# Kernel tuning notes

Measured on AMD Instinct MI355X. Metric: run time of the kernel, lower is better.

Reference implementation:

```python
import jax, jax.numpy as jnp
import numpy as np

VOCAB = 3149
T_MAX = 256
C = 128      # n_emb
H = 8        # n_heads
D = C // H   # head_size = 16
L = 6        # n blocks
FF = 4 * C
EPS = 1e-5


def _layernorm(x, g, b):
    mu = jnp.mean(x, axis=-1, keepdims=True)
    var = jnp.mean((x - mu) ** 2, axis=-1, keepdims=True)
    return (x - mu) / jnp.sqrt(var + EPS) * g + b


def setup_inputs() -> dict:
    key = jax.random.key(0)
    ks = jax.random.split(key, 24)
    s = 0.02
    inp = {
        "tokens": jax.random.randint(ks[0], (64, 256), 0, VOCAB),
        "tok_emb": jax.random.normal(ks[1], (VOCAB, C), jnp.float32) * s,
        "pos_emb": jax.random.normal(ks[2], (T_MAX, C), jnp.float32) * s,
        "Wq": jax.random.normal(ks[3], (L, H, C, D), jnp.float32) * s,
        "Wk": jax.random.normal(ks[4], (L, H, C, D), jnp.float32) * s,
        "Wv": jax.random.normal(ks[5], (L, H, C, D), jnp.float32) * s,
        "Wproj": jax.random.normal(ks[6], (L, C, C), jnp.float32) * s,
        "bproj": jnp.zeros((L, C), jnp.float32),
        "ln1_g": jnp.ones((L, C), jnp.float32),
        "ln1_b": jnp.zeros((L, C), jnp.float32),
        "ln2_g": jnp.ones((L, C), jnp.float32),
        "ln2_b": jnp.zeros((L, C), jnp.float32),
        "W1": jax.random.normal(ks[7], (L, C, FF), jnp.float32) * s,
        "b1": jnp.zeros((L, FF), jnp.float32),
        "W2": jax.random.normal(ks[8], (L, FF, C), jnp.float32) * s,
        "b2": jnp.zeros((L, C), jnp.float32),
        "lnf_g": jnp.ones((C,), jnp.float32),
        "lnf_b": jnp.zeros((C,), jnp.float32),
        "Wlm": jax.random.normal(ks[9], (C, VOCAB), jnp.float32) * s,
        "blm": jnp.zeros((VOCAB,), jnp.float32),
    }
    return inp


def reference(tokens, tok_emb, pos_emb, Wq, Wk, Wv, Wproj, bproj,
              ln1_g, ln1_b, ln2_g, ln2_b, W1, b1, W2, b2,
              lnf_g, lnf_b, Wlm, blm):
    B, T = tokens.shape
    x = tok_emb[tokens] + pos_emb[:T][None, :, :]  # (B,T,C)
    # NOTE: original code scales scores by C**-0.5 with C = n_emb (128), not head_size.
    scale = jnp.asarray(C, x.dtype) ** -0.5
    causal = jnp.tril(jnp.ones((T, T), bool))
    neg_inf = jnp.asarray(-jnp.inf, x.dtype)
    for l in range(L):
        xn = _layernorm(x, ln1_g[l], ln1_b[l])
        q = jnp.einsum('btc,hcd->bhtd', xn, Wq[l])
        k = jnp.einsum('btc,hcd->bhtd', xn, Wk[l])
        v = jnp.einsum('btc,hcd->bhtd', xn, Wv[l])
        wei = jnp.einsum('bhtd,bhsd->bhts', q, k) * scale
        wei = jnp.where(causal[None, None], wei, neg_inf)
        wei = jax.nn.softmax(wei, axis=-1)
        attn = jnp.einsum('bhts,bhsd->bhtd', wei, v)
        attn = attn.transpose(0, 2, 1, 3).reshape(B, T, C)  # concat heads
        x = x + jnp.einsum('btc,cf->btf', attn, Wproj[l]) + bproj[l]
        xn2 = _layernorm(x, ln2_g[l], ln2_b[l])
        h = jax.nn.relu(jnp.einsum('btc,cf->btf', xn2, W1[l]) + b1[l])
        x = x + jnp.einsum('btf,fc->btc', h, W2[l]) + b2[l]
    x = _layernorm(x, lnf_g, lnf_b)
    logits = jnp.einsum('btc,cv->btv', x, Wlm) + blm
    return logits
```

## Files before the change

kernel.cpp:

```cpp
#include <hip/hip_runtime.h>
#include <hip/hip_bf16.h>
#include <math.h>

#define BT   16384
#define CDIM 128
#define TSEQ 256
#define NBAT 64
#define NH   8
#define HD   16
#define NL   6
#define FFD  512
#define NV   3149

typedef __bf16 bfv8 __attribute__((ext_vector_type(8)));
typedef float  fv4  __attribute__((ext_vector_type(4)));
typedef short  s4   __attribute__((ext_vector_type(4)));
typedef unsigned short u16;
typedef unsigned int   u32;
typedef u16 u16v8 __attribute__((ext_vector_type(8)));

__device__ __forceinline__ u16 f2b(float f) {
  u32 u = __builtin_bit_cast(u32, f);
  u += 0x7FFFu + ((u >> 16) & 1u);
  return (u16)(u >> 16);
}
__device__ __forceinline__ u32 cvtpk(float lo, float hi) {
  u32 r;
  asm("v_cvt_pk_bf16_f32 %0, %1, %2" : "=v"(r) : "v"(lo), "v"(hi));
  return r;
}
__device__ __forceinline__ fv4 mfma16(s4 a, s4 b, fv4 c) {
#if __has_builtin(__builtin_amdgcn_mfma_f32_16x16x16bf16_1k)
  return __builtin_amdgcn_mfma_f32_16x16x16bf16_1k(a, b, c, 0, 0, 0);
#else
  fv4 d;
  asm volatile("v_mfma_f32_16x16x16_bf16 %0, %1, %2, %3"
               : "=v"(d) : "v"(a), "v"(b), "v"(c));
  return d;
#endif
}

__global__ __launch_bounds__(256) void embed_kernel(
    const int* __restrict__ tokens, const float* __restrict__ tok_emb,
    const float* __restrict__ pos_emb, float* __restrict__ x) {
  int i4 = blockIdx.x * 256 + threadIdx.x;
  if (i4 >= BT * CDIM / 4) return;
  int i  = i4 * 4;
  int c  = i & (CDIM - 1);
  int bt = i >> 7;
  int t  = bt & (TSEQ - 1);
  int tok = tokens[bt];
  float4 te = *(const float4*)(tok_emb + (size_t)tok * CDIM + c);
  float4 pe = *(const float4*)(pos_emb + (size_t)t * CDIM + c);
  float4 r;
  r.x = te.x + pe.x; r.y = te.y + pe.y; r.z = te.z + pe.z; r.w = te.w + pe.w;
  *(float4*)(x + i) = r;
}

__global__ __launch_bounds__(256) void packqkv_bf16(
    const float* __restrict__ Wq, const float* __restrict__ Wk,
    const float* __restrict__ Wv, u16* __restrict__ dst) {
  int idx = blockIdx.x * 256 + threadIdx.x;
  if (idx >= NL * 384 * CDIM) return;
  int c = idx & 127;
  int j = (idx >> 7) % 384;
  int l = idx / (384 * CDIM);
  int sel = j >> 7;
  int jj  = j & 127;
  int h   = jj >> 4;
  int d   = jj & 15;
  const float* W = (sel == 0) ? Wq : (sel == 1) ? Wk : Wv;
  dst[idx] = f2b(W[(((size_t)l * NH + h) * CDIM + c) * HD + d]);
}

__global__ __launch_bounds__(256) void transpose_cast_t(
    const float* __restrict__ src, u16* __restrict__ dst, int R, int C) {
  __shared__ float tile[32][33];
  int l  = blockIdx.z;
  int r0 = blockIdx.y * 32, c0 = blockIdx.x * 32;
  int tr = threadIdx.x >> 5, tc = threadIdx.x & 31;
  #pragma unroll
  for (int p = 0; p < 4; p++) {
    int r = r0 + tr + p * 8, c = c0 + tc;
    if (r < R && c < C) tile[tr + p * 8][tc] = src[((size_t)l * R + r) * C + c];
  }
  __syncthreads();
  #pragma unroll
  for (int p = 0; p < 4; p++) {
    int c = c0 + tr + p * 8, r = r0 + tc;
    if (r < R && c < C) dst[((size_t)l * C + c) * R + r] = f2b(tile[tc][tr + p * 8]);
  }
}

__global__ __launch_bounds__(256) void ln_kernel(
    const float* __restrict__ x, const float* __restrict__ g,
    const float* __restrict__ b, u16* __restrict__ out) {
  int wid  = blockIdx.x * 4 + (threadIdx.x >> 6);
  int lane = threadIdx.x & 63;
  const float2 v = ((const float2*)(x + (size_t)wid * CDIM))[lane];
  float s = v.x + v.y;
  #pragma unroll
  for (int m = 1; m < 64; m <<= 1) s += __shfl_xor(s, m);
  float mu = s * (1.f / CDIM);
  float dx = v.x - mu, dy = v.y - mu;
  float s2 = dx * dx + dy * dy;
  #pragma unroll
  for (int m = 1; m < 64; m <<= 1) s2 += __shfl_xor(s2, m);
  float rstd = rsqrtf(s2 * (1.f / CDIM) + 1e-5f);
  float2 gg = ((const float2*)g)[lane];
  float2 bb = ((const float2*)b)[lane];
  u32 pack = (u32)f2b(dx * rstd * gg.x + bb.x) |
             ((u32)f2b(dy * rstd * gg.y + bb.y) << 16);
  ((u32*)(out + (size_t)wid * CDIM))[lane] = pack;
}

template<int OMODE, bool BIAS, bool RELU, int BN>
__global__ __launch_bounds__(256) void gemm_mfma(
    const u16* __restrict__ A, const u16* __restrict__ Btp,
    const float* __restrict__ bias, void* __restrict__ Cout,
    int M, int N, int K) {
  constexpr int BM = 128, BK = 32, PAD = 40;
  constexpr int NF = BN / 32;
  __shared__ u16 As[BM][PAD];
  __shared__ u16 Bs[BN][PAD];
  const int tid  = threadIdx.x;
  const int lane = tid & 63;
  const int wv   = tid >> 6;
  const int wm   = wv & 1;
  const int wn   = wv >> 1;
  const int m0 = blockIdx.y * BM;
  const int n0 = blockIdx.x * BN;
  const int srow = tid >> 2;
  const int sk8  = (tid & 3) * 8;
  const int fr = lane & 15;
  const int fk = (lane >> 4) * 8;

  fv4 acc[4][NF];
  #pragma unroll
  for (int i = 0; i < 4; i++)
    #pragma unroll
    for (int j = 0; j < NF; j++) acc[i][j] = (fv4){0.f, 0.f, 0.f, 0.f};

  for (int k0 = 0; k0 < K; k0 += BK) {
    #pragma unroll
    for (int p = 0; p < 2; p++) {
      int r = srow + p * 64;
      *(uint4*)&As[r][sk8] = *(const uint4*)(A + (size_t)(m0 + r) * K + k0 + sk8);
    }
    #pragma unroll
    for (int p = 0; p < BN / 64; p++) {
      int r = srow + p * 64;
      int n = n0 + r;
      uint4 v = make_uint4(0u, 0u, 0u, 0u);
      if (n < N) v = *(const uint4*)(Btp + (size_t)n * K + k0 + sk8);
      *(uint4*)&Bs[r][sk8] = v;
    }
    __syncthreads();
    bfv8 a[4], b[NF];
    #pragma unroll
    for (int i = 0; i < 4; i++)
      a[i] = *(const bfv8*)&As[wm * 64 + i * 16 + fr][fk];
    #pragma unroll
    for (int j = 0; j < NF; j++)
      b[j] = *(const bfv8*)&Bs[wn * (BN / 2) + j * 16 + fr][fk];
    #pragma unroll
    for (int i = 0; i < 4; i++)
      #pragma unroll
      for (int j = 0; j < NF; j++)
        acc[i][j] = __builtin_amdgcn_mfma_f32_16x16x32_bf16(a[i], b[j], acc[i][j], 0, 0, 0);
    __syncthreads();
  }

  const int row0 = m0 + wm * 64;
  const int col0 = n0 + wn * (BN / 2);
  const int lr   = (lane >> 4) * 4;
  #pragma unroll
  for (int j = 0; j < NF; j++) {
    int col = col0 + j * 16 + fr;
    if (col >= N) continue;
    float bz = BIAS ? bias[col] : 0.f;
    #pragma unroll
    for (int i = 0; i < 4; i++) {
      #pragma unroll
      for (int q = 0; q < 4; q++) {
        int row = row0 + i * 16 + lr + q;
        float v = acc[i][j][q] + bz;
        if (RELU) v = fmaxf(v, 0.f);
        if (OMODE == 0)      ((u16*)Cout)[(size_t)row * N + col] = f2b(v);
        else if (OMODE == 1) ((float*)Cout)[(size_t)row * N + col] = v;
        else                 ((float*)Cout)[(size_t)row * N + col] += v;
      }
    }
  }
}

template<bool BIAS, bool RELU>
__global__ __launch_bounds__(256) void gemm_ln_mfma(
    const float* __restrict__ X, const u16* __restrict__ Btp,
    const float* __restrict__ lng, const float* __restrict__ lnb,
    const float* __restrict__ bias, u16* __restrict__ Cout,
    int M, int N) {
  constexpr int BM = 128, BN = 128, BK = 32;
  __shared__ u16 As[BM][136];
  __shared__ u16 Bs[BN][40];
  const int tid  = threadIdx.x;
  const int lane = tid & 63;
  const int wv   = tid >> 6;
  const int wm   = wv & 1;
  const int wn   = wv >> 1;
  const int m0 = blockIdx.y * BM;
  const int n0 = blockIdx.x * BN;
  const int fr = lane & 15;
  const int fk = (lane >> 4) * 8;

  {
    const int l32  = lane & 31;
    const int rsel = lane >> 5;
    float4 gg = *(const float4*)(lng + l32 * 4);
    float4 bb = *(const float4*)(lnb + l32 * 4);
    #pragma unroll 4
    for (int it = 0; it < 16; it++) {
      int r = wv * 32 + it * 2 + rsel;
      float4 v = *(const float4*)(X + (size_t)(m0 + r) * 128 + l32 * 4);
      float s = (v.x + v.y) + (v.z + v.w);
      #pragma unroll
      for (int m = 1; m < 32; m <<= 1) s += __shfl_xor(s, m);
      float mu = s * (1.f / 128.f);
      float dx = v.x - mu, dy = v.y - mu, dz = v.z - mu, dw = v.w - mu;
      float s2 = (dx * dx + dy * dy) + (dz * dz + dw * dw);
      #pragma unroll
      for (int m = 1; m < 32; m <<= 1) s2 += __shfl_xor(s2, m);
      float rstd = rsqrtf(s2 * (1.f / 128.f) + 1e-5f);
      u32 p0 = cvtpk(dx * rstd * gg.x + bb.x, dy * rstd * gg.y + bb.y);
      u32 p1 = cvtpk(dz * rstd * gg.z + bb.z, dw * rstd * gg.w + bb.w);
      *(uint2*)&As[r][l32 * 4] = make_uint2(p0, p1);
    }
  }

  fv4 acc[4][4];
  #pragma unroll
  for (int i = 0; i < 4; i++)
    #pragma unroll
    for (int j = 0; j < 4; j++) acc[i][j] = (fv4){0.f, 0.f, 0.f, 0.f};

  for (int k0 = 0; k0 < 128; k0 += BK) {
    #pragma unroll
    for (int p = 0; p < 2; p++) {
      int ch = tid + p * 256;
      int row = ch >> 2, c8 = (ch & 3) * 8;
      *(uint4*)&Bs[row][c8] = *(const uint4*)(Btp + (size_t)(n0 + row) * 128 + k0 + c8);
    }
    __syncthreads();
    bfv8 a[4], b[4];
    #pragma unroll
    for (int i = 0; i < 4; i++)
      a[i] = *(const bfv8*)&As[wm * 64 + i * 16 + fr][k0 + fk];
    #pragma unroll
    for (int j = 0; j < 4; j++)
      b[j] = *(const bfv8*)&Bs[wn * 64 + j * 16 + fr][fk];
    #pragma unroll
    for (int i = 0; i < 4; i++)
      #pragma unroll
      for (int j = 0; j < 4; j++)
        acc[i][j] = __builtin_amdgcn_mfma_f32_16x16x32_bf16(a[i], b[j], acc[i][j], 0, 0, 0);
    __syncthreads();
  }

  const int row0 = m0 + wm * 64;
  const int col0 = n0 + wn * 64;
  const int lr   = (lane >> 4) * 4;
  #pragma unroll
  for (int j = 0; j < 4; j++) {
    int col = col0 + j * 16 + fr;
    float bz = BIAS ? bias[col] : 0.f;
    #pragma unroll
    for (int i = 0; i < 4; i++) {
      #pragma unroll
      for (int q = 0; q < 4; q++) {
        int row = row0 + i * 16 + lr + q;
        float v = acc[i][j][q] + bz;
        if (RELU) v = fmaxf(v, 0.f);
        Cout[(size_t)row * N + col] = f2b(v);
      }
    }
  }
}

__global__ __launch_bounds__(256) void attn_mfma(
    const u16* __restrict__ qkv, u16* __restrict__ out) {
  const float scale = 0.08838834764831843f;
  __shared__ u16 Qs[128][20];
  __shared__ u16 Ks[TSEQ][20];
  __shared__ u16 Vt[HD][280];
  const int blk = blockIdx.x;
  const int qh = blk & 1;
  const int h  = (blk >> 1) & (NH - 1);
  const int b  = blk >> 4;
  const int tid = threadIdx.x;

  #pragma unroll
  for (int p = 0; p < 2; p++) {
    int idx = tid + p * 256;
    int r  = idx >> 1;
    int c8 = (idx & 1) * 8;
    const u16* base = qkv + (size_t)(b * TSEQ + r) * 384 + h * HD + c8;
    uint4 k  = *(const uint4*)(base + CDIM);
    u16v8 v  = *(const u16v8*)(base + 2 * CDIM);
    *(uint4*)&Ks[r][c8] = k;
    #pragma unroll
    for (int i = 0; i < 8; i++) Vt[c8 + i][r] = v[i];
  }
  {
    int r  = tid >> 1;
    int c8 = (tid & 1) * 8;
    const u16* base = qkv + (size_t)(b * TSEQ + qh * 128 + r) * 384 + h * HD + c8;
    *(uint4*)&Qs[r][c8] = *(const uint4*)(base);
  }
  __syncthreads();

  const int wv   = tid >> 6;
  const int lane = tid & 63;
  const int fr = lane & 15;
  const int g  = lane >> 4;

  #pragma unroll 1
  for (int qi = 0; qi < 2; qi++) {
    const int qt = qh * 8 + (qi ? (7 - wv) : wv);
    const int qr = (qt - qh * 8) * 16 + fr;
    s4 qf = *(const s4*)&Qs[qr][g * 4];

    fv4 sf[16];
    #pragma unroll
    for (int st = 0; st < 16; st++) {
      if (st <= qt) {
        s4 kf = *(const s4*)&Ks[st * 16 + fr][g * 4];
        sf[st] = mfma16(kf, qf, (fv4){0.f, 0.f, 0.f, 0.f});
      }
    }

    float mx = -3.4e38f;
    #pragma unroll
    for (int st = 0; st < 16; st++) {
      if (st <= qt) {
        #pragma unroll
        for (int r = 0; r < 4; r++) {
          float v = sf[st][r] * scale;
          if (st == qt && (4 * g + r) > fr) v = -3.4e38f;
          sf[st][r] = v;
          mx = fmaxf(mx, v);
        }
      }
    }
    mx = fmaxf(mx, __shfl_xor(mx, 16));
    mx = fmaxf(mx, __shfl_xor(mx, 32));

    float sum = 0.f;
    uint2 pk[16];
    #pragma unroll
    for (int st = 0; st < 16; st++) {
      if (st <= qt) {
        float e0 = __expf(sf[st][0] - mx), e1 = __expf(sf[st][1] - mx);
        float e2 = __expf(sf[st][2] - mx), e3 = __expf(sf[st][3] - mx);
        sum += (e0 + e1) + (e2 + e3);
        pk[st] = make_uint2(cvtpk(e0, e1), cvtpk(e2, e3));
      }
    }
    sum += __shfl_xor(sum, 16);
    sum += __shfl_xor(sum, 32);
    const float inv = 1.f / sum;

    fv4 accO = (fv4){0.f, 0.f, 0.f, 0.f};
    #pragma unroll
    for (int st = 0; st < 16; st++) {
      if (st <= qt) {
        s4 vf = *(const s4*)&Vt[fr][st * 16 + g * 4];
        s4 pf = __builtin_bit_cast(s4, pk[st]);
        accO = mfma16(vf, pf, accO);
      }
    }

    const int q_glob = qt * 16 + fr;
    u32 lo = cvtpk(accO[0] * inv, accO[1] * inv);
    u32 hi = cvtpk(accO[2] * inv, accO[3] * inv);
    *(uint2*)(out + (size_t)(b * TSEQ + q_glob) * CDIM + h * HD + 4 * g) =
        make_uint2(lo, hi);
  }
}

extern "C" void kernel_launch(void* const* d_in, const int* in_sizes, int n_in,
                              void* d_out, int out_size, void* d_ws, size_t ws_size,
                              hipStream_t stream) {
  const int*   tokens  = (const int*)  d_in[0];
  const float* tok_emb = (const float*)d_in[1];
  const float* pos_emb = (const float*)d_in[2];
  const float* Wq      = (const float*)d_in[3];
  const float* Wk      = (const float*)d_in[4];
  const float* Wv      = (const float*)d_in[5];
  const float* Wproj   = (const float*)d_in[6];
  const float* bproj   = (const float*)d_in[7];
  const float* ln1_g   = (const float*)d_in[8];
  const float* ln1_b   = (const float*)d_in[9];
  const float* ln2_g   = (const float*)d_in[10];
  const float* ln2_b   = (const float*)d_in[11];
  const float* W1      = (const float*)d_in[12];
  const float* b1      = (const float*)d_in[13];
  const float* W2      = (const float*)d_in[14];
  const float* b2      = (const float*)d_in[15];
  const float* lnf_g   = (const float*)d_in[16];
  const float* lnf_b   = (const float*)d_in[17];
  const float* Wlm     = (const float*)d_in[18];
  const float* blm     = (const float*)d_in[19];
  float* out = (float*)d_out;

  char* W = (char*)d_ws;
  float* x    = (float*)(W);
  u16*   xn   = (u16*)  (W + 8388608);
  u16*   qkvb = (u16*)  (W + 12582912);
  u16*   att  = (u16*)  (W + 25165824);
  u16*   hbuf = (u16*)  (W + 29360128);
  u16*   wqkv = (u16*)  (W + 46137344);
  u16*   wpj  = (u16*)  (W + 46727168);
  u16*   w1t  = (u16*)  (W + 46923776);
  u16*   w2t  = (u16*)  (W + 47710208);
  u16*   wlmt = (u16*)  (W + 48496640);

  packqkv_bf16<<<(NL * 384 * CDIM + 255) / 256, 256, 0, stream>>>(Wq, Wk, Wv, wqkv);
  transpose_cast_t<<<dim3(4, 4, NL), 256, 0, stream>>>(Wproj, wpj, CDIM, CDIM);
  transpose_cast_t<<<dim3(16, 4, NL), 256, 0, stream>>>(W1, w1t, CDIM, FFD);
  transpose_cast_t<<<dim3(4, 16, NL), 256, 0, stream>>>(W2, w2t, FFD, CDIM);
  transpose_cast_t<<<dim3((NV + 31) / 32, 4, 1), 256, 0, stream>>>(Wlm, wlmt, CDIM, NV);
  embed_kernel<<<(BT * CDIM / 4 + 255) / 256, 256, 0, stream>>>(tokens, tok_emb, pos_emb, x);

  for (int l = 0; l < NL; l++) {
    gemm_ln_mfma<false, false><<<dim3(3, BT / 128), 256, 0, stream>>>(
        x, wqkv + (size_t)l * 384 * CDIM, ln1_g + l * CDIM, ln1_b + l * CDIM,
        nullptr, qkvb, BT, 384);
    attn_mfma<<<NBAT * NH * 2, 256, 0, stream>>>(qkvb, att);
    gemm_mfma<2, true, false, 64><<<dim3(2, BT / 128), 256, 0, stream>>>(
        att, wpj + (size_t)l * CDIM * CDIM, bproj + l * CDIM, x, BT, CDIM, CDIM);
    gemm_ln_mfma<true, true><<<dim3(4, BT / 128), 256, 0, stream>>>(
        x, w1t + (size_t)l * FFD * CDIM, ln2_g + l * CDIM, ln2_b + l * CDIM,
        b1 + l * FFD, hbuf, BT, FFD);
    gemm_mfma<2, true, false, 64><<<dim3(2, BT / 128), 256, 0, stream>>>(
        hbuf, w2t + (size_t)l * CDIM * FFD, b2 + l * CDIM, x, BT, CDIM, FFD);
  }
  ln_kernel<<<BT / 4, 256, 0, stream>>>(x, lnf_g, lnf_b, xn);
  gemm_mfma<1, true, false, 128><<<dim3((NV + 127) / 128, BT / 128), 256, 0, stream>>>(
      xn, wlmt, blm, out, BT, NV, CDIM);
}
```

Baseline: 847.4 us.

## Fuse final layernorm into LM head, shrink GEMM row tiles, use online-softmax attention

The final layernorm kernel is removed and folded into the LM-head GEMM through a generalized gemm_ln_mfma that can write float output and handles ragged N. The per-layer GEMMs switch from 128-row to 64-row tiles, doubling the block count for better CU occupancy. Attention replaces the two-pass softmax over a 16-tile score array with a streaming online-softmax loop, which lowers register pressure at the cost of extra rescaling and shuffles per tile. The V-transpose shared array padding is also changed to alter bank mapping.

Measured after the change: 758.3 us. 10.5% less time.

```diff
diff --git a/kernel.cpp b/kernel.cpp
--- a/kernel.cpp
+++ b/kernel.cpp
@@ -92,34 +92,13 @@
   }
 }
 
-__global__ __launch_bounds__(256) void ln_kernel(
-    const float* __restrict__ x, const float* __restrict__ g,
-    const float* __restrict__ b, u16* __restrict__ out) {
-  int wid  = blockIdx.x * 4 + (threadIdx.x >> 6);
-  int lane = threadIdx.x & 63;
-  const float2 v = ((const float2*)(x + (size_t)wid * CDIM))[lane];
-  float s = v.x + v.y;
-  #pragma unroll
-  for (int m = 1; m < 64; m <<= 1) s += __shfl_xor(s, m);
-  float mu = s * (1.f / CDIM);
-  float dx = v.x - mu, dy = v.y - mu;
-  float s2 = dx * dx + dy * dy;
-  #pragma unroll
-  for (int m = 1; m < 64; m <<= 1) s2 += __shfl_xor(s2, m);
-  float rstd = rsqrtf(s2 * (1.f / CDIM) + 1e-5f);
-  float2 gg = ((const float2*)g)[lane];
-  float2 bb = ((const float2*)b)[lane];
-  u32 pack = (u32)f2b(dx * rstd * gg.x + bb.x) |
-             ((u32)f2b(dy * rstd * gg.y + bb.y) << 16);
-  ((u32*)(out + (size_t)wid * CDIM))[lane] = pack;
-}
-
-template<int OMODE, bool BIAS, bool RELU, int BN>
+template<int OMODE, bool BIAS, bool RELU, int BM, int BN>
 __global__ __launch_bounds__(256) void gemm_mfma(
     const u16* __restrict__ A, const u16* __restrict__ Btp,
     const float* __restrict__ bias, void* __restrict__ Cout,
     int M, int N, int K) {
-  constexpr int BM = 128, BK = 32, PAD = 40;
+  constexpr int BK = 32, PAD = 40;
+  constexpr int MI = BM / 32;
   constexpr int NF = BN / 32;
   __shared__ u16 As[BM][PAD];
   __shared__ u16 Bs[BN][PAD];
@@ -135,15 +114,15 @@
   const int fr = lane & 15;
   const int fk = (lane >> 4) * 8;
 
-  fv4 acc[4][NF];
-  #pragma unroll
-  for (int i = 0; i < 4; i++)
+  fv4 acc[MI][NF];
+  #pragma unroll
+  for (int i = 0; i < MI; i++)
     #pragma unroll
     for (int j = 0; j < NF; j++) acc[i][j] = (fv4){0.f, 0.f, 0.f, 0.f};
 
   for (int k0 = 0; k0 < K; k0 += BK) {
     #pragma unroll
-    for (int p = 0; p < 2; p++) {
+    for (int p = 0; p < BM / 64; p++) {
       int r = srow + p * 64;
       *(uint4*)&As[r][sk8] = *(const uint4*)(A + (size_t)(m0 + r) * K + k0 + sk8);
     }
@@ -156,22 +135,22 @@
       *(uint4*)&Bs[r][sk8] = v;
     }
     __syncthreads();
-    bfv8 a[4], b[NF];
-    #pragma unroll
-    for (int i = 0; i < 4; i++)
-      a[i] = *(const bfv8*)&As[wm * 64 + i * 16 + fr][fk];
+    bfv8 a[MI], b[NF];
+    #pragma unroll
+    for (int i = 0; i < MI; i++)
+      a[i] = *(const bfv8*)&As[wm * (BM / 2) + i * 16 + fr][fk];
     #pragma unroll
     for (int j = 0; j < NF; j++)
       b[j] = *(const bfv8*)&Bs[wn * (BN / 2) + j * 16 + fr][fk];
     #pragma unroll
-    for (int i = 0; i < 4; i++)
+    for (int i = 0; i < MI; i++)
       #pragma unroll
       for (int j = 0; j < NF; j++)
         acc[i][j] = __builtin_amdgcn_mfma_f32_16x16x32_bf16(a[i], b[j], acc[i][j], 0, 0, 0);
     __syncthreads();
   }
 
-  const int row0 = m0 + wm * 64;
+  const int row0 = m0 + wm * (BM / 2);
   const int col0 = n0 + wn * (BN / 2);
   const int lr   = (lane >> 4) * 4;
   #pragma unroll
@@ -180,7 +159,7 @@
     if (col >= N) continue;
     float bz = BIAS ? bias[col] : 0.f;
     #pragma unroll
-    for (int i = 0; i < 4; i++) {
+    for (int i = 0; i < MI; i++) {
       #pragma unroll
       for (int q = 0; q < 4; q++) {
         int row = row0 + i * 16 + lr + q;
@@ -194,13 +173,15 @@
   }
 }
 
-template<bool BIAS, bool RELU>
+template<int OMODE, bool BIAS, bool RELU, int BM, int BN>
 __global__ __launch_bounds__(256) void gemm_ln_mfma(
     const float* __restrict__ X, const u16* __restrict__ Btp,
     const float* __restrict__ lng, const float* __restrict__ lnb,
-    const float* __restrict__ bias, u16* __restrict__ Cout,
+    const float* __restrict__ bias, void* __restrict__ Cout,
     int M, int N) {
-  constexpr int BM = 128, BN = 128, BK = 32;
+  constexpr int BK = 32;
+  constexpr int MI = BM / 32;
+  constexpr int NF = BN / 32;
   __shared__ u16 As[BM][136];
   __shared__ u16 Bs[BN][40];
   const int tid  = threadIdx.x;
@@ -218,9 +199,9 @@
     const int rsel = lane >> 5;
     float4 gg = *(const float4*)(lng + l32 * 4);
     float4 bb = *(const float4*)(lnb + l32 * 4);
-    #pragma unroll 4
-    for (int it = 0; it < 16; it++) {
-      int r = wv * 32 + it * 2 + rsel;
+    #pragma unroll 2
+    for (int it = 0; it < BM / 8; it++) {
+      int r = it * 8 + wv * 2 + rsel;
       float4 v = *(const float4*)(X + (size_t)(m0 + r) * 128 + l32 * 4);
       float s = (v.x + v.y) + (v.z + v.w);
       #pragma unroll
@@ -237,50 +218,55 @@
     }
   }
 
-  fv4 acc[4][4];
-  #pragma unroll
-  for (int i = 0; i < 4; i++)
-    #pragma unroll
-    for (int j = 0; j < 4; j++) acc[i][j] = (fv4){0.f, 0.f, 0.f, 0.f};
+  fv4 acc[MI][NF];
+  #pragma unroll
+  for (int i = 0; i < MI; i++)
+    #pragma unroll
+    for (int j = 0; j < NF; j++) acc[i][j] = (fv4){0.f, 0.f, 0.f, 0.f};
 
   for (int k0 = 0; k0 < 128; k0 += BK) {
     #pragma unroll
-    for (int p = 0; p < 2; p++) {
+    for (int p = 0; p < BN / 64; p++) {
       int ch = tid + p * 256;
       int row = ch >> 2, c8 = (ch & 3) * 8;
-      *(uint4*)&Bs[row][c8] = *(const uint4*)(Btp + (size_t)(n0 + row) * 128 + k0 + c8);
+      int n = n0 + row;
+      uint4 v = make_uint4(0u, 0u, 0u, 0u);
+      if (n < N) v = *(const uint4*)(Btp + (size_t)n * 128 + k0 + c8);
+      *(uint4*)&Bs[row][c8] = v;
     }
     __syncthreads();
-    bfv8 a[4], b[4];
-    #pragma unroll
-    for (int i = 0; i < 4; i++)
-      a[i] = *(const bfv8*)&As[wm * 64 + i * 16 + fr][k0 + fk];
-    #pragma unroll
-    for (int j = 0; j < 4; j++)
-      b[j] = *(const bfv8*)&Bs[wn * 64 + j * 16 + fr][fk];
-    #pragma unroll
-    for (int i = 0; i < 4; i++)
-      #pragma unroll
-      for (int j = 0; j < 4; j++)
+    bfv8 a[MI], b[NF];
+    #pragma unroll
+    for (int i = 0; i < MI; i++)
+      a[i] = *(const bfv8*)&As[wm * (BM / 2) + i * 16 + fr][k0 + fk];
+    #pragma unroll
+    for (int j = 0; j < NF; j++)
+      b[j] = *(const bfv8*)&Bs[wn * (BN / 2) + j * 16 + fr][fk];
+    #pragma unroll
+    for (int i = 0; i < MI; i++)
+      #pragma unroll
+      for (int j = 0; j < NF; j++)
         acc[i][j] = __builtin_amdgcn_mfma_f32_16x16x32_bf16(a[i], b[j], acc[i][j], 0, 0, 0);
     __syncthreads();
   }
 
-  const int row0 = m0 + wm * 64;
-  const int col0 = n0 + wn * 64;
+  const int row0 = m0 + wm * (BM / 2);
+  const int col0 = n0 + wn * (BN / 2);
   const int lr   = (lane >> 4) * 4;
   #pragma unroll
-  for (int j = 0; j < 4; j++) {
+  for (int j = 0; j < NF; j++) {
     int col = col0 + j * 16 + fr;
+    if (col >= N) continue;
     float bz = BIAS ? bias[col] : 0.f;
     #pragma unroll
-    for (int i = 0; i < 4; i++) {
+    for (int i = 0; i < MI; i++) {
       #pragma unroll
       for (int q = 0; q < 4; q++) {
         int row = row0 + i * 16 + lr + q;
         float v = acc[i][j][q] + bz;
         if (RELU) v = fmaxf(v, 0.f);
-        Cout[(size_t)row * N + col] = f2b(v);
+        if (OMODE == 0) ((u16*)Cout)[(size_t)row * N + col] = f2b(v);
+        else            ((float*)Cout)[(size_t)row * N + col] = v;
       }
     }
   }
@@ -291,7 +277,7 @@
   const float scale = 0.08838834764831843f;
   __shared__ u16 Qs[128][20];
   __shared__ u16 Ks[TSEQ][20];
-  __shared__ u16 Vt[HD][280];
+  __shared__ u16 Vt[HD][284];
   const int blk = blockIdx.x;
   const int qh = blk & 1;
   const int h  = (blk >> 1) & (NH - 1);
@@ -326,58 +312,58 @@
   #pragma unroll 1
   for (int qi = 0; qi < 2; qi++) {
     const int qt = qh * 8 + (qi ? (7 - wv) : wv);
-    const int qr = (qt - qh * 8) * 16 + fr;
-    s4 qf = *(const s4*)&Qs[qr][g * 4];
-
-    fv4 sf[16];
-    #pragma unroll
-    for (int st = 0; st < 16; st++) {
-      if (st <= qt) {
-        s4 kf = *(const s4*)&Ks[st * 16 + fr][g * 4];
-        sf[st] = mfma16(kf, qf, (fv4){0.f, 0.f, 0.f, 0.f});
-      }
-    }
-
-    float mx = -3.4e38f;
-    #pragma unroll
-    for (int st = 0; st < 16; st++) {
-      if (st <= qt) {
-        #pragma unroll
-        for (int r = 0; r < 4; r++) {
-          float v = sf[st][r] * scale;
-          if (st == qt && (4 * g + r) > fr) v = -3.4e38f;
-          sf[st][r] = v;
-          mx = fmaxf(mx, v);
-        }
-      }
-    }
-    mx = fmaxf(mx, __shfl_xor(mx, 16));
-    mx = fmaxf(mx, __shfl_xor(mx, 32));
-
-    float sum = 0.f;
-    uint2 pk[16];
-    #pragma unroll
-    for (int st = 0; st < 16; st++) {
-      if (st <= qt) {
-        float e0 = __expf(sf[st][0] - mx), e1 = __expf(sf[st][1] - mx);
-        float e2 = __expf(sf[st][2] - mx), e3 = __expf(sf[st][3] - mx);
-        sum += (e0 + e1) + (e2 + e3);
-        pk[st] = make_uint2(cvtpk(e0, e1), cvtpk(e2, e3));
-      }
-    }
-    sum += __shfl_xor(sum, 16);
-    sum += __shfl_xor(sum, 32);
-    const float inv = 1.f / sum;
-
+    s4 qf = *(const s4*)&Qs[(qt & 7) * 16 + fr][g * 4];
+
+    float m = -3.4e38f, l = 0.f;
     fv4 accO = (fv4){0.f, 0.f, 0.f, 0.f};
-    #pragma unroll
-    for (int st = 0; st < 16; st++) {
-      if (st <= qt) {
-        s4 vf = *(const s4*)&Vt[fr][st * 16 + g * 4];
-        s4 pf = __builtin_bit_cast(s4, pk[st]);
-        accO = mfma16(vf, pf, accO);
-      }
-    }
+
+    for (int st = 0; st < qt; st++) {
+      s4 kf = *(const s4*)&Ks[st * 16 + fr][g * 4];
+      fv4 sc = mfma16(kf, qf, (fv4){0.f, 0.f, 0.f, 0.f});
+      float s0 = sc[0] * scale, s1 = sc[1] * scale;
+      float s2 = sc[2] * scale, s3 = sc[3] * scale;
+      float tm = fmaxf(fmaxf(s0, s1), fmaxf(s2, s3));
+      tm = fmaxf(tm, __shfl_xor(tm, 16));
+      tm = fmaxf(tm, __shfl_xor(tm, 32));
+      float mn = fmaxf(m, tm);
+      float corr = __expf(m - mn);
+      float e0 = __expf(s0 - mn), e1 = __expf(s1 - mn);
+      float e2 = __expf(s2 - mn), e3 = __expf(s3 - mn);
+      l = l * corr + (e0 + e1) + (e2 + e3);
+      accO[0] *= corr; accO[1] *= corr; accO[2] *= corr; accO[3] *= corr;
+      s4 pf = __builtin_bit_cast(s4, make_uint2(cvtpk(e0, e1), cvtpk(e2, e3)));
+      s4 vf = *(const s4*)&Vt[fr][st * 16 + g * 4];
+      accO = mfma16(vf, pf, accO);
+      m = mn;
+    }
+    {
+      s4 kf = *(const s4*)&Ks[qt * 16 + fr][g * 4];
+      fv4 sc = mfma16(kf, qf, (fv4){0.f, 0.f, 0.f, 0.f});
+      const float NEG = -3.4e38f;
+      float s0 = (4 * g + 0 > fr) ? NEG : sc[0] * scale;
+      float s1 = (4 * g + 1 > fr) ? NEG : sc[1] * scale;
+      float s2 = (4 * g + 2 > fr) ? NEG : sc[2] * scale;
+      float s3 = (4 * g + 3 > fr) ? NEG : sc[3] * scale;
+      float tm = fmaxf(fmaxf(s0, s1), fmaxf(s2, s3));
+      tm = fmaxf(tm, __shfl_xor(tm, 16));
+      tm = fmaxf(tm, __shfl_xor(tm, 32));
+      float mn = fmaxf(m, tm);
+      float corr = __expf(m - mn);
+      float e0 = (s0 <= -1e37f) ? 0.f : __expf(s0 - mn);
+      float e1 = (s1 <= -1e37f) ? 0.f : __expf(s1 - mn);
+      float e2 = (s2 <= -1e37f) ? 0.f : __expf(s2 - mn);
+      float e3 = (s3 <= -1e37f) ? 0.f : __expf(s3 - mn);
+      l = l * corr + (e0 + e1) + (e2 + e3);
+      accO[0] *= corr; accO[1] *= corr; accO[2] *= corr; accO[3] *= corr;
+      s4 pf = __builtin_bit_cast(s4, make_uint2(cvtpk(e0, e1), cvtpk(e2, e3)));
+      s4 vf = *(const s4*)&Vt[fr][qt * 16 + g * 4];
+      accO = mfma16(vf, pf, accO);
+    }
+
+    float lt = l;
+    lt += __shfl_xor(lt, 16);
+    lt += __shfl_xor(lt, 32);
+    const float inv = 1.f / lt;
 
     const int q_glob = qt * 16 + fr;
     u32 lo = cvtpk(accO[0] * inv, accO[1] * inv);
@@ -414,7 +400,6 @@
 
   char* W = (char*)d_ws;
   float* x    = (float*)(W);
-  u16*   xn   = (u16*)  (W + 8388608);
   u16*   qkvb = (u16*)  (W + 12582912);
   u16*   att  = (u16*)  (W + 25165824);
   u16*   hbuf = (u16*)  (W + 29360128);
@@ -432,19 +417,18 @@
   embed_kernel<<<(BT * CDIM / 4 + 255) / 256, 256, 0, stream>>>(tokens, tok_emb, pos_emb, x);
 
   for (int l = 0; l < NL; l++) {
-    gemm_ln_mfma<false, false><<<dim3(3, BT / 128), 256, 0, stream>>>(
+    gemm_ln_mfma<0, false, false, 64, 128><<<dim3(3, BT / 64), 256, 0, stream>>>(
         x, wqkv + (size_t)l * 384 * CDIM, ln1_g + l * CDIM, ln1_b + l * CDIM,
         nullptr, qkvb, BT, 384);
     attn_mfma<<<NBAT * NH * 2, 256, 0, stream>>>(qkvb, att);
-    gemm_mfma<2, true, false, 64><<<dim3(2, BT / 128), 256, 0, stream>>>(
+    gemm_mfma<2, true, false, 64, 64><<<dim3(2, BT / 64), 256, 0, stream>>>(
         att, wpj + (size_t)l * CDIM * CDIM, bproj + l * CDIM, x, BT, CDIM, CDIM);
-    gemm_ln_mfma<true, true><<<dim3(4, BT / 128), 256, 0, stream>>>(
+    gemm_ln_mfma<0, true, true, 64, 128><<<dim3(4, BT / 64), 256, 0, stream>>>(
         x, w1t + (size_t)l * FFD * CDIM, ln2_g + l * CDIM, ln2_b + l * CDIM,
         b1 + l * FFD, hbuf, BT, FFD);
-    gemm_mfma<2, true, false, 64><<<dim3(2, BT / 128), 256, 0, stream>>>(
+    gemm_mfma<2, true, false, 64, 64><<<dim3(2, BT / 64), 256, 0, stream>>>(
         hbuf, w2t + (size_t)l * CDIM * FFD, b2 + l * CDIM, x, BT, CDIM, FFD);
   }
-  ln_kernel<<<BT / 4, 256, 0, stream>>>(x, lnf_g, lnf_b, xn);
-  gemm_mfma<1, true, false, 128><<<dim3((NV + 127) / 128, BT / 128), 256, 0, stream>>>(
-      xn, wlmt, blm, out, BT, NV, CDIM);
-}
+  gemm_ln_mfma<1, true, false, 128, 128><<<dim3((NV + 127) / 128, BT / 128), 256, 0, stream>>>(
+      x, wlmt, lnf_g, lnf_b, blm, out, BT, NV);
+}
```
